# Kernel optimization log

Hardware: AMD Instinct MI355X
Metric: run time of the kernel (lower is better)

## Reference

```python
import jax, jax.numpy as jnp
import numpy as np

B, C_IN, T, H, W = 4, 256, 8, 56, 56
C_OUT = 256
KT, KH, KW = 1, 3, 3
PH, PW = 1, 1
SH, SW = 1, 1


def setup_inputs() -> dict:
    key = jax.random.key(0)
    k1, k2, k3, k4 = jax.random.split(key, 4)
    x = jax.random.normal(k1, (B, C_IN, T, H, W), dtype=jnp.float32)
    alpha = jax.random.normal(k2, (B, C_IN, T, 1, 1), dtype=jnp.float32)
    # base weight: torch shape (1,1,c_out,c_in//g,kt,kh,kw); store squeezed
    fan_in = C_IN * KT * KH * KW
    bound_w = float(np.sqrt(6.0 / fan_in))  # kaiming_uniform a=sqrt(5) -> U(-sqrt(6/fan_in), +)
    weight = jax.random.uniform(k3, (C_OUT, C_IN, KT, KH, KW), dtype=jnp.float32,
                                minval=-bound_w, maxval=bound_w)
    bound_b = float(1.0 / np.sqrt(fan_in))
    bias = jax.random.uniform(k4, (C_OUT,), dtype=jnp.float32, minval=-bound_b, maxval=bound_b)
    return {"x": x, "alpha": alpha, "weight": weight, "bias": bias}


def reference(x, alpha, weight, bias):
    b, c_in, t, h, w = x.shape
    c_out, _, kt, kh, kw = weight.shape
    pad_t = kt // 2
    # temporal unfold: pad t by kt//2 on both sides, gather kt-wide windows
    xp = jnp.pad(x, ((0, 0), (0, 0), (pad_t, pad_t), (0, 0), (0, 0)))
    idx = jnp.arange(t)[:, None] + jnp.arange(kt)[None, :]  # (t, kt)
    xu = xp[:, :, idx]                                      # (b, c_in, t, kt, h, w)
    xu = jnp.transpose(xu, (0, 2, 1, 3, 4, 5)).reshape(b * t, c_in, kt, h, w)
    # per-frame weights: W_t = alpha_t * W_base  (cal_dim='cin' -> alpha scales c_in axis)
    a = jnp.transpose(alpha[..., 0, 0], (0, 2, 1))          # (b, t, c_in)
    wts = a[:, :, None, :, None, None, None] * weight[None, None]  # (b, t, c_out, c_in, kt, kh, kw)
    wts = wts.reshape(b * t, c_out, c_in, kt, kh, kw)

    def conv_one(xi, wi):
        # xi: (c_in, kt, h, w), wi: (c_out, c_in, kt, kh, kw)
        o = jax.lax.conv_general_dilated(
            xi[None], wi,
            window_strides=(1, SH, SW),
            padding=((0, 0), (PH, PH), (PW, PW)),
            dimension_numbers=('NCDHW', 'OIDHW', 'NCDHW'))
        return o[0, :, 0]  # (c_out, h_out, w_out); depth collapses to 1

    out = jax.vmap(conv_one)(xu, wts)                       # (b*t, c_out, h_out, w_out)
    out = out + bias[None, :, None, None]
    h_out, w_out = out.shape[-2], out.shape[-1]
    out = out.reshape(b, t, c_out, h_out, w_out).transpose(0, 2, 1, 3, 4)
    return out
```

## Files before the change

### kernel.cpp

```cpp
#include <hip/hip_runtime.h>
#include <hip/hip_bf16.h>

typedef __attribute__((ext_vector_type(8))) short short8;
typedef __attribute__((ext_vector_type(4))) float floatx4;

#define C_INN 256
#define T_N   8
#define H_N   56
#define W_N   56
#define C_OUTN 256
#define HW_N  (H_N * W_N)
#define THW   (T_N * HW_N)
#define NTAP  9
#define LDX_S 40

#define GLOAD_LDS16(gp, lp) \
  __builtin_amdgcn_global_load_lds((const __attribute__((address_space(1))) void*)(gp), \
                                   (__attribute__((address_space(3))) void*)(lp), 16, 0, 0)

__global__ void prep_weight(const float* __restrict__ w, __hip_bfloat16* __restrict__ wb) {
    int idx = blockIdx.x * blockDim.x + threadIdx.x;
    if (idx >= C_OUTN * NTAP * C_INN) return;
    int e    = idx & 7;
    int c    = (idx >> 3) % 2304;
    int g4   = (idx >> 3) / 2304;
    int r    = c & 63;
    int tq   = c >> 6;
    int quad = tq & 3, tap = tq >> 2;
    int cg = g4 >> 2, mtile = g4 & 3;
    int o  = mtile * 64 + r;
    int ci = cg * 32 + quad * 8 + e;
    wb[idx] = __float2bfloat16(w[(o * C_INN + ci) * NTAP + tap]);
}

__global__ __launch_bounds__(256, 2) void tada_conv(
    const float* __restrict__ x, const float* __restrict__ alpha,
    const __hip_bfloat16* __restrict__ wb, const float* __restrict__ bias,
    float* __restrict__ out)
{
    __shared__ __hip_bfloat16 lA[2304 * 8];
    __shared__ __hip_bfloat16 lX[340 * LDX_S];

    const int tid = threadIdx.x;

    const int id  = blockIdx.x;
    const int nid = (id & 7) * 224 + (id >> 3);
    const int mtile = nid & 3;
    const int ntile = (nid >> 2) % 14;
    const int bt    = nid / 56;
    const int b = bt >> 3, t = bt & 7;
    const int h0 = (ntile % 7) * 8;
    const int w0 = (ntile / 7) * 32;

    const int wn   = tid >> 6;
    const int lane = tid & 63;
    const int col = lane & 15, quad = lane >> 4;

    const int cil4 = tid & 3;
    const int pxl  = tid >> 2;

    int xoff[6];
#pragma unroll
    for (int it = 0; it < 6; ++it) {
        int px = pxl + it * 64;
        int hi = px / 34;
        int wi = px - hi * 34;
        int hh = h0 - 1 + hi;
        int ww = w0 - 1 + wi;
        bool inimg = (px < 340) && ((unsigned)hh < (unsigned)H_N) && ((unsigned)ww < (unsigned)W_N);
        xoff[it] = inimg ? (hh * W_N + ww) : -1;
    }

    floatx4 acc[4][4];
#pragma unroll
    for (int i = 0; i < 4; ++i)
#pragma unroll
        for (int j = 0; j < 4; ++j)
            acc[i][j] = (floatx4){0.f, 0.f, 0.f, 0.f};

    const long xbase = ((long)b * C_INN) * THW + (long)t * HW_N;
    const int  abase = b * C_INN * T_N + t;

    float pX[6][8];
    float pa[8];

    auto PREFETCH = [&](int cgp) {
        const int ci0 = cgp * 32 + cil4 * 8;
#pragma unroll
        for (int j = 0; j < 8; ++j)
            pa[j] = alpha[abase + (ci0 + j) * T_N];
        const float* xc = x + xbase + (long)ci0 * THW;
#pragma unroll
        for (int it = 0; it < 6; ++it) {
            if (xoff[it] >= 0) {
                const float* xp = xc + xoff[it];
#pragma unroll
                for (int j = 0; j < 8; ++j)
                    pX[it][j] = xp[j * THW];
            } else {
#pragma unroll
                for (int j = 0; j < 8; ++j)
                    pX[it][j] = 0.f;
            }
        }
    };

    PREFETCH(0);

    for (int cg = 0; cg < 8; ++cg) {
        __syncthreads();

        {
            const __hip_bfloat16* wsrc = wb + ((long)(cg * 4 + mtile) * 2304) * 8;
            const int cb = wn * 64;
#pragma unroll
            for (int it = 0; it < 9; ++it) {
                GLOAD_LDS16(wsrc + (long)(it * 256 + cb + lane) * 8,
                            (char*)lA + (it * 256 + cb) * 16);
            }
        }

#pragma unroll
        for (int it = 0; it < 6; ++it) {
            int px = pxl + it * 64;
            if (it < 5 || pxl < 20) {
                union { __hip_bfloat16 h[8]; short8 v; } pk;
#pragma unroll
                for (int j = 0; j < 8; ++j)
                    pk.h[j] = __float2bfloat16(pX[it][j] * pa[j]);
                *reinterpret_cast<short8*>(&lX[px * LDX_S + cil4 * 8]) = pk.v;
            }
        }

        __syncthreads();

        if (cg < 7) PREFETCH(cg + 1);

        const __hip_bfloat16* lAr = lA + quad * 512 + col * 8;
#pragma unroll
        for (int kh = 0; kh < 3; ++kh) {
#pragma unroll
            for (int kw = 0; kw < 3; ++kw) {
                const int tap = kh * 3 + kw;
                short8 af[4], bf[4];
#pragma unroll
                for (int mi = 0; mi < 4; ++mi)
                    af[mi] = *(const short8*)(lAr + tap * 2048 + mi * 128);
#pragma unroll
                for (int ni = 0; ni < 4; ++ni) {
                    int g  = wn * 4 + ni;
                    int px = ((g >> 1) + kh) * 34 + (g & 1) * 16 + col + kw;
                    bf[ni] = *(const short8*)(lX + px * LDX_S + quad * 8);
                }
#pragma unroll
                for (int mi = 0; mi < 4; ++mi)
#pragma unroll
                    for (int ni = 0; ni < 4; ++ni)
                        acc[mi][ni] = __builtin_amdgcn_mfma_f32_16x16x32_bf16(
                            af[mi], bf[ni], acc[mi][ni], 0, 0, 0);
            }
        }
    }

#pragma unroll
    for (int mi = 0; mi < 4; ++mi) {
        const floatx4 bv = *(const floatx4*)(bias + mtile * 64 + mi * 16 + quad * 4);
#pragma unroll
        for (int ni = 0; ni < 4; ++ni) {
            int n  = wn * 64 + ni * 16 + col;
            int ph = n >> 5, pw = n & 31;
            if (w0 + pw < W_N) {
#pragma unroll
                for (int r = 0; r < 4; ++r) {
                    int m = mtile * 64 + mi * 16 + quad * 4 + r;
                    out[(((long)b * C_OUTN + m) * T_N + t) * HW_N + (h0 + ph) * W_N + (w0 + pw)]
                        = acc[mi][ni][r] + bv[r];
                }
            }
        }
    }
}

extern "C" void kernel_launch(void* const* d_in, const int* in_sizes, int n_in,
                              void* d_out, int out_size, void* d_ws, size_t ws_size,
                              hipStream_t stream) {
    const float* x      = (const float*)d_in[0];
    const float* alpha  = (const float*)d_in[1];
    const float* weight = (const float*)d_in[2];
    const float* bias   = (const float*)d_in[3];
    float* out = (float*)d_out;

    __hip_bfloat16* wb = (__hip_bfloat16*)d_ws;

    int nprep = C_OUTN * NTAP * C_INN;
    prep_weight<<<(nprep + 255) / 256, 256, 0, stream>>>(weight, wb);

    tada_conv<<<dim3(1792), 256, 0, stream>>>(x, alpha, wb, bias, out);
}
```

Measured before the change: 358.7 us.

## Read weights directly from global memory and drop register prefetch to raise occupancy

```diff
diff --git a/kernel.cpp b/kernel.cpp
--- a/kernel.cpp
+++ b/kernel.cpp
@@ -14,10 +14,6 @@
 #define NTAP  9
 #define LDX_S 40
 
-#define GLOAD_LDS16(gp, lp) \
-  __builtin_amdgcn_global_load_lds((const __attribute__((address_space(1))) void*)(gp), \
-                                   (__attribute__((address_space(3))) void*)(lp), 16, 0, 0)
-
 __global__ void prep_weight(const float* __restrict__ w, __hip_bfloat16* __restrict__ wb) {
     int idx = blockIdx.x * blockDim.x + threadIdx.x;
     if (idx >= C_OUTN * NTAP * C_INN) return;
@@ -33,12 +29,11 @@
     wb[idx] = __float2bfloat16(w[(o * C_INN + ci) * NTAP + tap]);
 }
 
-__global__ __launch_bounds__(256, 2) void tada_conv(
+__global__ __launch_bounds__(256, 4) void tada_conv(
     const float* __restrict__ x, const float* __restrict__ alpha,
     const __hip_bfloat16* __restrict__ wb, const float* __restrict__ bias,
     float* __restrict__ out)
 {
-    __shared__ __hip_bfloat16 lA[2304 * 8];
     __shared__ __hip_bfloat16 lX[340 * LDX_S];
 
     const int tid = threadIdx.x;
@@ -81,62 +76,41 @@
     const long xbase = ((long)b * C_INN) * THW + (long)t * HW_N;
     const int  abase = b * C_INN * T_N + t;
 
-    float pX[6][8];
-    float pa[8];
-
-    auto PREFETCH = [&](int cgp) {
-        const int ci0 = cgp * 32 + cil4 * 8;
-#pragma unroll
-        for (int j = 0; j < 8; ++j)
-            pa[j] = alpha[abase + (ci0 + j) * T_N];
-        const float* xc = x + xbase + (long)ci0 * THW;
-#pragma unroll
-        for (int it = 0; it < 6; ++it) {
-            if (xoff[it] >= 0) {
-                const float* xp = xc + xoff[it];
-#pragma unroll
-                for (int j = 0; j < 8; ++j)
-                    pX[it][j] = xp[j * THW];
-            } else {
-#pragma unroll
-                for (int j = 0; j < 8; ++j)
-                    pX[it][j] = 0.f;
-            }
-        }
-    };
-
-    PREFETCH(0);
+    const __hip_bfloat16* wq = wb + ((long)mtile * 2304 + quad * 64 + col) * 8;
+    const __hip_bfloat16* lXw = lX + wn * 2720 + col * 40 + quad * 8;
 
     for (int cg = 0; cg < 8; ++cg) {
         __syncthreads();
 
         {
-            const __hip_bfloat16* wsrc = wb + ((long)(cg * 4 + mtile) * 2304) * 8;
-            const int cb = wn * 64;
+            const int ci0 = cg * 32 + cil4 * 8;
+            float a[8];
 #pragma unroll
-            for (int it = 0; it < 9; ++it) {
-                GLOAD_LDS16(wsrc + (long)(it * 256 + cb + lane) * 8,
-                            (char*)lA + (it * 256 + cb) * 16);
+            for (int j = 0; j < 8; ++j)
+                a[j] = alpha[abase + (ci0 + j) * T_N];
+            const float* xc = x + xbase + (long)ci0 * THW;
+#pragma unroll
+            for (int it = 0; it < 6; ++it) {
+                int px = pxl + it * 64;
+                if (it < 5 || pxl < 20) {
+                    union { __hip_bfloat16 h[8]; short8 v; } pk;
+                    if (xoff[it] >= 0) {
+                        const float* xp = xc + xoff[it];
+#pragma unroll
+                        for (int j = 0; j < 8; ++j)
+                            pk.h[j] = __float2bfloat16(xp[j * THW] * a[j]);
+                    } else {
+#pragma unroll
+                        for (int j = 0; j < 8; ++j)
+                            pk.h[j] = __float2bfloat16(0.f);
+                    }
+                    *reinterpret_cast<short8*>(&lX[px * LDX_S + cil4 * 8]) = pk.v;
+                }
             }
         }
-
-#pragma unroll
-        for (int it = 0; it < 6; ++it) {
-            int px = pxl + it * 64;
-            if (it < 5 || pxl < 20) {
-                union { __hip_bfloat16 h[8]; short8 v; } pk;
-#pragma unroll
-                for (int j = 0; j < 8; ++j)
-                    pk.h[j] = __float2bfloat16(pX[it][j] * pa[j]);
-                *reinterpret_cast<short8*>(&lX[px * LDX_S + cil4 * 8]) = pk.v;
-            }
-        }
-
         __syncthreads();
 
-        if (cg < 7) PREFETCH(cg + 1);
-
-        const __hip_bfloat16* lAr = lA + quad * 512 + col * 8;
+        const __hip_bfloat16* wcg = wq + (long)cg * 4 * 2304 * 8;
 #pragma unroll
         for (int kh = 0; kh < 3; ++kh) {
 #pragma unroll
@@ -145,13 +119,11 @@
                 short8 af[4], bf[4];
 #pragma unroll
                 for (int mi = 0; mi < 4; ++mi)
-                    af[mi] = *(const short8*)(lAr + tap * 2048 + mi * 128);
+                    af[mi] = *(const short8*)(wcg + (tap * 256 + mi * 16) * 8);
 #pragma unroll
-                for (int ni = 0; ni < 4; ++ni) {
-                    int g  = wn * 4 + ni;
-                    int px = ((g >> 1) + kh) * 34 + (g & 1) * 16 + col + kw;
-                    bf[ni] = *(const short8*)(lX + px * LDX_S + quad * 8);
-                }
+                for (int ni = 0; ni < 4; ++ni)
+                    bf[ni] = *(const short8*)(lXw + ((ni >> 1) + kh) * 1360
+                                                  + (ni & 1) * 640 + kw * 40);
 #pragma unroll
                 for (int mi = 0; mi < 4; ++mi)
 #pragma unroll
```

Result: slower. 434.8 us (+21.2%).

## Load weight fragments directly from global memory and double-buffer MFMA operands

Applied to the files above, without the earlier changes.

```diff
diff --git a/kernel.cpp b/kernel.cpp
--- a/kernel.cpp
+++ b/kernel.cpp
@@ -13,10 +13,6 @@
 #define THW   (T_N * HW_N)
 #define NTAP  9
 #define LDX_S 40
-
-#define GLOAD_LDS16(gp, lp) \
-  __builtin_amdgcn_global_load_lds((const __attribute__((address_space(1))) void*)(gp), \
-                                   (__attribute__((address_space(3))) void*)(lp), 16, 0, 0)
 
 __global__ void prep_weight(const float* __restrict__ w, __hip_bfloat16* __restrict__ wb) {
     int idx = blockIdx.x * blockDim.x + threadIdx.x;
@@ -38,7 +34,6 @@
     const __hip_bfloat16* __restrict__ wb, const float* __restrict__ bias,
     float* __restrict__ out)
 {
-    __shared__ __hip_bfloat16 lA[2304 * 8];
     __shared__ __hip_bfloat16 lX[340 * LDX_S];
 
     const int tid = threadIdx.x;
@@ -81,6 +76,9 @@
     const long xbase = ((long)b * C_INN) * THW + (long)t * HW_N;
     const int  abase = b * C_INN * T_N + t;
 
+    const __hip_bfloat16* wq = wb + ((long)mtile * 2304 + quad * 64 + col) * 8;
+    const __hip_bfloat16* lXw = lX + wn * 2720 + col * 40 + quad * 8;
+
     float pX[6][8];
     float pa[8];
 
@@ -110,16 +108,6 @@
     for (int cg = 0; cg < 8; ++cg) {
         __syncthreads();
 
-        {
-            const __hip_bfloat16* wsrc = wb + ((long)(cg * 4 + mtile) * 2304) * 8;
-            const int cb = wn * 64;
-#pragma unroll
-            for (int it = 0; it < 9; ++it) {
-                GLOAD_LDS16(wsrc + (long)(it * 256 + cb + lane) * 8,
-                            (char*)lA + (it * 256 + cb) * 16);
-            }
-        }
-
 #pragma unroll
         for (int it = 0; it < 6; ++it) {
             int px = pxl + it * 64;
@@ -131,34 +119,38 @@
                 *reinterpret_cast<short8*>(&lX[px * LDX_S + cil4 * 8]) = pk.v;
             }
         }
-
         __syncthreads();
 
         if (cg < 7) PREFETCH(cg + 1);
 
-        const __hip_bfloat16* lAr = lA + quad * 512 + col * 8;
+        const __hip_bfloat16* wcg = wq + (long)cg * 73728;
+        short8 af[2][4], bf[2][4];
 #pragma unroll
-        for (int kh = 0; kh < 3; ++kh) {
+        for (int mi = 0; mi < 4; ++mi)
+            af[0][mi] = *(const short8*)(wcg + (mi * 16) * 8);
 #pragma unroll
-            for (int kw = 0; kw < 3; ++kw) {
-                const int tap = kh * 3 + kw;
-                short8 af[4], bf[4];
+        for (int ni = 0; ni < 4; ++ni)
+            bf[0][ni] = *(const short8*)(lXw + (ni >> 1) * 1360 + (ni & 1) * 640);
+
+#pragma unroll
+        for (int tap = 0; tap < 9; ++tap) {
+            const int cur = tap & 1, nxt = cur ^ 1;
+            if (tap < 8) {
+                const int tn = tap + 1, khn = tn / 3, kwn = tn % 3;
 #pragma unroll
                 for (int mi = 0; mi < 4; ++mi)
-                    af[mi] = *(const short8*)(lAr + tap * 2048 + mi * 128);
+                    af[nxt][mi] = *(const short8*)(wcg + (tn * 256 + mi * 16) * 8);
 #pragma unroll
-                for (int ni = 0; ni < 4; ++ni) {
-                    int g  = wn * 4 + ni;
-                    int px = ((g >> 1) + kh) * 34 + (g & 1) * 16 + col + kw;
-                    bf[ni] = *(const short8*)(lX + px * LDX_S + quad * 8);
-                }
+                for (int ni = 0; ni < 4; ++ni)
+                    bf[nxt][ni] = *(const short8*)(lXw + ((ni >> 1) + khn) * 1360
+                                                       + (ni & 1) * 640 + kwn * 40);
+            }
 #pragma unroll
-                for (int mi = 0; mi < 4; ++mi)
+            for (int mi = 0; mi < 4; ++mi)
 #pragma unroll
-                    for (int ni = 0; ni < 4; ++ni)
-                        acc[mi][ni] = __builtin_amdgcn_mfma_f32_16x16x32_bf16(
-                            af[mi], bf[ni], acc[mi][ni], 0, 0, 0);
-            }
+                for (int ni = 0; ni < 4; ++ni)
+                    acc[mi][ni] = __builtin_amdgcn_mfma_f32_16x16x32_bf16(
+                        af[cur][mi], bf[cur][ni], acc[mi][ni], 0, 0, 0);
         }
     }
 
```

Measured after the change: 533.6 us. 1.49x slower.

## Pre-scale and transpose input to channel-last bf16 in a separate prep kernel

Applied to the files above, without the earlier changes.

```diff
diff --git a/kernel.cpp b/kernel.cpp
--- a/kernel.cpp
+++ b/kernel.cpp
@@ -13,6 +13,9 @@
 #define THW   (T_N * HW_N)
 #define NTAP  9
 #define LDX_S 40
+
+#define XS_OFF  2097152
+#define XS_BYTES ((long)32 * HW_N * C_INN * 2)
 
 #define GLOAD_LDS16(gp, lp) \
   __builtin_amdgcn_global_load_lds((const __attribute__((address_space(1))) void*)(gp), \
@@ -33,8 +36,44 @@
     wb[idx] = __float2bfloat16(w[(o * C_INN + ci) * NTAP + tap]);
 }
 
+__global__ void prep_xs(const float* __restrict__ x, const float* __restrict__ alpha,
+                        __hip_bfloat16* __restrict__ xs) {
+    __shared__ __hip_bfloat16 ls[64][72];
+    const int pt = blockIdx.x;
+    const int ct = blockIdx.y;
+    const int bt = blockIdx.z;
+    const int b = bt >> 3, t = bt & 7;
+    const int px0 = pt * 64, ci0 = ct * 64;
+    const int tid = threadIdx.x;
+    const int r = tid >> 6, l = tid & 63;
+
+    const float* xb = x + (long)b * (C_INN * THW) + (long)t * HW_N;
+    const float* ab = alpha + b * (C_INN * T_N) + t;
+#pragma unroll
+    for (int rr2 = 0; rr2 < 8; ++rr2) {
+        int c0 = r * 16 + rr2 * 2;
+        int ci = ci0 + c0;
+        float v0 = xb[(long)ci * THW + px0 + l]       * ab[ci * T_N];
+        float v1 = xb[(long)(ci + 1) * THW + px0 + l] * ab[(ci + 1) * T_N];
+        union { __hip_bfloat16 h[2]; unsigned u; } pk;
+        pk.h[0] = __float2bfloat16(v0);
+        pk.h[1] = __float2bfloat16(v1);
+        *reinterpret_cast<unsigned*>(&ls[l][c0]) = pk.u;
+    }
+    __syncthreads();
+#pragma unroll
+    for (int p = 0; p < 2; ++p) {
+        int pxl = (tid >> 3) + p * 32;
+        int ch  = tid & 7;
+        short8 v = *reinterpret_cast<const short8*>(&ls[pxl][ch * 8]);
+        *reinterpret_cast<short8*>(xs + ((long)bt * HW_N + px0 + pxl) * C_INN + ci0 + ch * 8) = v;
+    }
+}
+
+template<int PRE>
 __global__ __launch_bounds__(256, 2) void tada_conv(
     const float* __restrict__ x, const float* __restrict__ alpha,
+    const __hip_bfloat16* __restrict__ xs,
     const __hip_bfloat16* __restrict__ wb, const float* __restrict__ bias,
     float* __restrict__ out)
 {
@@ -81,26 +120,49 @@
     const long xbase = ((long)b * C_INN) * THW + (long)t * HW_N;
     const int  abase = b * C_INN * T_N + t;
 
-    float pX[6][8];
-    float pa[8];
+    const __hip_bfloat16* lAr = lA + quad * 512 + col * 8;
+    const __hip_bfloat16* lXw = lX + wn * 2720 + col * 40 + quad * 8;
+
+    short8 pXv[6];
+    float  pX[6][8];
+    float  pa[8];
+    const short8 ZV = {0, 0, 0, 0, 0, 0, 0, 0};
+
+    long boff[6];
+    if constexpr (PRE) {
+#pragma unroll
+        for (int it = 0; it < 6; ++it)
+            boff[it] = (xoff[it] >= 0)
+                ? ((long)bt * HW_N + xoff[it]) * (C_INN * 2) + cil4 * 16
+                : -1;
+    }
 
     auto PREFETCH = [&](int cgp) {
-        const int ci0 = cgp * 32 + cil4 * 8;
-#pragma unroll
-        for (int j = 0; j < 8; ++j)
-            pa[j] = alpha[abase + (ci0 + j) * T_N];
-        const float* xc = x + xbase + (long)ci0 * THW;
-#pragma unroll
-        for (int it = 0; it < 6; ++it) {
-            if (xoff[it] >= 0) {
-                const float* xp = xc + xoff[it];
-#pragma unroll
-                for (int j = 0; j < 8; ++j)
-                    pX[it][j] = xp[j * THW];
-            } else {
-#pragma unroll
-                for (int j = 0; j < 8; ++j)
-                    pX[it][j] = 0.f;
+        if constexpr (PRE) {
+#pragma unroll
+            for (int it = 0; it < 6; ++it)
+                pXv[it] = (boff[it] >= 0)
+                    ? *reinterpret_cast<const short8*>(
+                          reinterpret_cast<const char*>(xs) + boff[it] + (long)cgp * 64)
+                    : ZV;
+        } else {
+            const int ci0 = cgp * 32 + cil4 * 8;
+#pragma unroll
+            for (int j = 0; j < 8; ++j)
+                pa[j] = alpha[abase + (ci0 + j) * T_N];
+            const float* xc = x + xbase + (long)ci0 * THW;
+#pragma unroll
+            for (int it = 0; it < 6; ++it) {
+                if (xoff[it] >= 0) {
+                    const float* xp = xc + xoff[it];
+#pragma unroll
+                    for (int j = 0; j < 8; ++j)
+                        pX[it][j] = xp[j * THW];
+                } else {
+#pragma unroll
+                    for (int j = 0; j < 8; ++j)
+                        pX[it][j] = 0.f;
+                }
             }
         }
     };
@@ -124,19 +186,21 @@
         for (int it = 0; it < 6; ++it) {
             int px = pxl + it * 64;
             if (it < 5 || pxl < 20) {
-                union { __hip_bfloat16 h[8]; short8 v; } pk;
-#pragma unroll
-                for (int j = 0; j < 8; ++j)
-                    pk.h[j] = __float2bfloat16(pX[it][j] * pa[j]);
-                *reinterpret_cast<short8*>(&lX[px * LDX_S + cil4 * 8]) = pk.v;
-            }
-        }
-
+                if constexpr (PRE) {
+                    *reinterpret_cast<short8*>(&lX[px * LDX_S + cil4 * 8]) = pXv[it];
+                } else {
+                    union { __hip_bfloat16 h[8]; short8 v; } pk;
+#pragma unroll
+                    for (int j = 0; j < 8; ++j)
+                        pk.h[j] = __float2bfloat16(pX[it][j] * pa[j]);
+                    *reinterpret_cast<short8*>(&lX[px * LDX_S + cil4 * 8]) = pk.v;
+                }
+            }
+        }
         __syncthreads();
 
         if (cg < 7) PREFETCH(cg + 1);
 
-        const __hip_bfloat16* lAr = lA + quad * 512 + col * 8;
 #pragma unroll
         for (int kh = 0; kh < 3; ++kh) {
 #pragma unroll
@@ -147,11 +211,9 @@
                 for (int mi = 0; mi < 4; ++mi)
                     af[mi] = *(const short8*)(lAr + tap * 2048 + mi * 128);
 #pragma unroll
-                for (int ni = 0; ni < 4; ++ni) {
-                    int g  = wn * 4 + ni;
-                    int px = ((g >> 1) + kh) * 34 + (g & 1) * 16 + col + kw;
-                    bf[ni] = *(const short8*)(lX + px * LDX_S + quad * 8);
-                }
+                for (int ni = 0; ni < 4; ++ni)
+                    bf[ni] = *(const short8*)(lXw + ((ni >> 1) + kh) * 1360
+                                                  + (ni & 1) * 640 + kw * 40);
 #pragma unroll
                 for (int mi = 0; mi < 4; ++mi)
 #pragma unroll
@@ -195,5 +257,11 @@
     int nprep = C_OUTN * NTAP * C_INN;
     prep_weight<<<(nprep + 255) / 256, 256, 0, stream>>>(weight, wb);
 
-    tada_conv<<<dim3(1792), 256, 0, stream>>>(x, alpha, wb, bias, out);
-}
+    if (ws_size >= (size_t)(XS_OFF + XS_BYTES)) {
+        __hip_bfloat16* xsb = (__hip_bfloat16*)((char*)d_ws + XS_OFF);
+        prep_xs<<<dim3(49, 4, 32), 256, 0, stream>>>(x, alpha, xsb);
+        tada_conv<1><<<dim3(1792), 256, 0, stream>>>(x, alpha, xsb, wb, bias, out);
+    } else {
+        tada_conv<0><<<dim3(1792), 256, 0, stream>>>(x, alpha, nullptr, wb, bias, out);
+    }
+}
```

Result: faster. 319.7 us (-10.9%).
